# Performance work log

Hardware: AMD Instinct MI355X
Metric: run time of the kernel (lower is better)

The kernel has to match this reference:

```python
import jax, jax.numpy as jnp
import numpy as np

MARGIN = 0.3
EPS = 1e-8


def setup_inputs() -> dict:
    key = jax.random.key(0)
    k1, k2 = jax.random.split(key)
    B, D, NUM_IDS = 8192, 128, 1024
    embeddings = jax.random.normal(k1, (B, D), dtype=jnp.float32)
    labels = jax.random.randint(k2, (B,), 0, NUM_IDS, dtype=jnp.int64)
    return {"embeddings": embeddings, "labels": labels}


def _pairwise_distance(embeddings):
    # dist[i,j] = sqrt(relu(||e_i||^2 - 2 e_i.e_j + ||e_j||^2) + eps)
    dot = embeddings @ embeddings.T                       # [B, B]
    sq = jnp.diagonal(dot)                                # [B]
    d2 = sq[None, :] - 2.0 * dot + sq[:, None]
    return jnp.sqrt(jax.nn.relu(d2) + EPS)


def reference(embeddings, labels):
    B = labels.shape[0]
    dist = _pairwise_distance(embeddings)                 # [B, B]

    same = labels[:, None] == labels[None, :]             # [B, B]
    eye = jnp.eye(B, dtype=bool)
    pos_mask = same & ~eye
    neg_mask = ~same

    neg_inf = jnp.finfo(dist.dtype).min
    pos_inf = jnp.finfo(dist.dtype).max
    hardest_pos = jnp.max(jnp.where(pos_mask, dist, neg_inf), axis=1)  # [B]
    hardest_neg = jnp.min(jnp.where(neg_mask, dist, pos_inf), axis=1)  # [B]

    valid = pos_mask.any(axis=1) & neg_mask.any(axis=1)   # [B]
    per_anchor = jax.nn.relu(hardest_pos - hardest_neg + MARGIN)
    loss_sum = jnp.sum(jnp.where(valid, per_anchor, 0.0))
    n_triplets = jnp.sum(valid)
    return loss_sum / jnp.maximum(n_triplets, 1).astype(loss_sum.dtype)
```

## Files before the change

kernel.cpp:

```cpp
#include <hip/hip_runtime.h>

#define BSZ 8192
#define DIM 128
#define NLAB 1024
#define MARGIN 0.3f
#define EPS 1e-8f
#define NJ 32
#define JCHUNK 256
#define NPH 8

typedef __bf16 bf16x8 __attribute__((ext_vector_type(8)));
typedef float f32x4 __attribute__((ext_vector_type(4)));

#define AS1 __attribute__((address_space(1)))
#define AS3 __attribute__((address_space(3)))

__device__ __forceinline__ unsigned enc_ord(float f) {
    unsigned u = __float_as_uint(f);
    return (u & 0x80000000u) ? ~u : (u | 0x80000000u);
}
__device__ __forceinline__ float dec_ord(unsigned e) {
    unsigned u = (e & 0x80000000u) ? (e & 0x7FFFFFFFu) : ~e;
    return __uint_as_float(u);
}

template <int N>
__device__ __forceinline__ void waitv() {
    if constexpr (N == 4) asm volatile("s_waitcnt vmcnt(4)" ::: "memory");
    else if constexpr (N == 2) asm volatile("s_waitcnt vmcnt(2)" ::: "memory");
    else asm volatile("s_waitcnt vmcnt(0)" ::: "memory");
}

__global__ __launch_bounds__(1024) void k_sort(const int* __restrict__ labels,
                                               unsigned* __restrict__ start,
                                               unsigned* __restrict__ offset) {
    __shared__ unsigned h[NLAB];
    const int tid = threadIdx.x;
    h[tid] = 0u;
    __syncthreads();
#pragma unroll
    for (int s = 0; s < BSZ / NLAB; ++s)
        atomicAdd(&h[labels[s * NLAB + tid]], 1u);
    __syncthreads();
    for (int d = 1; d < NLAB; d <<= 1) {
        unsigned w = (tid >= d) ? h[tid - d] : 0u;
        __syncthreads();
        h[tid] += w;
        __syncthreads();
    }
    start[tid + 1] = h[tid];
    if (tid == 0) start[0] = 0u;
    offset[tid] = (tid > 0) ? h[tid - 1] : 0u;
}

__global__ __launch_bounds__(256) void k_scatter(const int* __restrict__ labels,
                                                 unsigned* __restrict__ offset,
                                                 int* __restrict__ perm,
                                                 int* __restrict__ slab) {
    int i = blockIdx.x * 256 + threadIdx.x;
    int lab = labels[i];
    unsigned pos = atomicAdd(&offset[lab], 1u);
    perm[pos] = i;
    slab[pos] = lab;
}

__global__ __launch_bounds__(256) void k_prep(const float* __restrict__ emb,
                                              const int* __restrict__ perm,
                                              __bf16* __restrict__ hi,
                                              float* __restrict__ sq,
                                              unsigned* __restrict__ maxp,
                                              unsigned* __restrict__ minn,
                                              float* __restrict__ sumcnt) {
    int row = blockIdx.x * 4 + (threadIdx.x >> 6);
    int lane = threadIdx.x & 63;
    int src = perm[row];
    float2 v = *(const float2*)&emb[(size_t)src * DIM + lane * 2];
    union { __bf16 b[2]; unsigned u; } p;
    p.b[0] = (__bf16)v.x;
    p.b[1] = (__bf16)v.y;
    ((unsigned*)hi)[row * 64 + lane] = p.u;
    float s = v.x * v.x + v.y * v.y;
#pragma unroll
    for (int m = 32; m >= 1; m >>= 1) s += __shfl_xor(s, m);
    if (lane == 0) {
        sq[row] = s;
        maxp[row] = 0u;
        minn[row] = 0xFFFFFFFFu;
    }
    if (blockIdx.x == 0 && threadIdx.x == 0) {
        sumcnt[0] = 0.0f;
        ((unsigned*)sumcnt)[1] = 0u;
    }
}

__global__ __launch_bounds__(256, 4) void k_mfma(const __bf16* __restrict__ hi,
                                                 const int* __restrict__ slab,
                                                 const unsigned* __restrict__ startp,
                                                 const float* __restrict__ sq,
                                                 unsigned* __restrict__ maxp,
                                                 unsigned* __restrict__ minn) {
    __shared__ char Bst[4][8][1024];
    __shared__ float sqlds[JCHUNK];
    __shared__ int lablds[JCHUNK];

    const int tid = threadIdx.x;
    const int lane = tid & 63;
    const int wave = tid >> 6;
    const int lr = lane & 15;
    const int lq = lane >> 4;
    const int i0 = blockIdx.x * 128;
    const int it0 = i0 + wave * 32;
    const int it1 = it0 + 16;
    const int j0 = blockIdx.y * JCHUNK;
    const float INF = __uint_as_float(0x7F800000u);

    const int lf = slab[i0];
    const int ll = slab[i0 + 127];
    const int blo = (int)startp[lf];
    const int bhi = (int)startp[ll + 1];
    unsigned mmask = 0;
#pragma unroll
    for (int tt = 0; tt < NPH; ++tt) {
        int c0 = j0 + tt * 32;
        if (bhi > c0 && blo < c0 + 32) mmask |= (1u << tt);
    }

    sqlds[tid] = sq[j0 + tid];
    lablds[tid] = slab[j0 + tid];

    bf16x8 a0[4], a1[4];
    const __bf16* ap = hi + (size_t)(it0 + lr) * DIM + lq * 8;
#pragma unroll
    for (int f = 0; f < 4; ++f) {
        a0[f] = *(const bf16x8*)&ap[f * 32];
        a1[f] = *(const bf16x8*)&ap[16 * DIM + f * 32];
        asm volatile("" : "+v"(a0[f]));
        asm volatile("" : "+v"(a1[f]));
    }
    const int4 li0 = *(const int4*)&slab[it0 + lq * 4];
    const int4 li1 = *(const int4*)&slab[it1 + lq * 4];
    const int labi0[4] = {li0.x, li0.y, li0.z, li0.w};
    const int labi1[4] = {li1.x, li1.y, li1.z, li1.w};

    float mp0[4], mp1[4], mn0[4], mn1[4];
#pragma unroll
    for (int r = 0; r < 4; ++r) {
        mp0[r] = -INF; mp1[r] = -INF;
        mn0[r] = INF;  mn1[r] = INF;
    }

    const int m0 = wave * 2, m1 = m0 + 1;
    const __bf16* bsA = hi + (size_t)(j0 + (m0 >> 2) * 16 + lr) * DIM + (m0 & 3) * 32 + lq * 8;
    const __bf16* bsB = hi + (size_t)(j0 + (m1 >> 2) * 16 + lr) * DIM + (m1 & 3) * 32 + lq * 8;
#define STAGE(t, buf)                                                              \
    do {                                                                           \
        __builtin_amdgcn_global_load_lds(                                          \
            (const AS1 void*)(bsA + (size_t)(t) * 32 * DIM),                       \
            (AS3 void*)&Bst[buf][m0][0], 16, 0, 0);                                \
        __builtin_amdgcn_global_load_lds(                                          \
            (const AS1 void*)(bsB + (size_t)(t) * 32 * DIM),                       \
            (AS3 void*)&Bst[buf][m1][0], 16, 0, 0);                                \
    } while (0)

    STAGE(0, 0);
    STAGE(1, 1);
    __syncthreads();

#pragma unroll 1
    for (int t = 0; t < NPH; ++t) {
        if (t + 2 < NPH) STAGE(t + 2, (t + 2) & 3);
        if (t < NPH - 2) waitv<4>();
        else if (t == NPH - 2) waitv<2>();
        else waitv<0>();
        __builtin_amdgcn_s_barrier();
        __builtin_amdgcn_sched_barrier(0);

        const float sqj0 = sqlds[t * 32 + lr];
        const float sqj1 = sqlds[t * 32 + 16 + lr];

        const bf16x8* bp = (const bf16x8*)&Bst[t & 3][0][0];
        f32x4 acc00 = {0, 0, 0, 0}, acc01 = {0, 0, 0, 0};
        f32x4 acc10 = {0, 0, 0, 0}, acc11 = {0, 0, 0, 0};
#pragma unroll
        for (int f = 0; f < 4; ++f) {
            bf16x8 b0 = bp[f * 64 + lane];
            bf16x8 b1 = bp[(4 + f) * 64 + lane];
            acc00 = __builtin_amdgcn_mfma_f32_16x16x32_bf16(a0[f], b0, acc00, 0, 0, 0);
            acc10 = __builtin_amdgcn_mfma_f32_16x16x32_bf16(a1[f], b0, acc10, 0, 0, 0);
            acc01 = __builtin_amdgcn_mfma_f32_16x16x32_bf16(a0[f], b1, acc01, 0, 0, 0);
            acc11 = __builtin_amdgcn_mfma_f32_16x16x32_bf16(a1[f], b1, acc11, 0, 0, 0);
        }

        if (mmask & (1u << t)) {
            const int labj0 = lablds[t * 32 + lr];
            const int labj1 = lablds[t * 32 + 16 + lr];
#pragma unroll
            for (int r = 0; r < 4; ++r) {
                float k00 = fmaf(-2.0f, acc00[r], sqj0);
                float k01 = fmaf(-2.0f, acc01[r], sqj1);
                float k10 = fmaf(-2.0f, acc10[r], sqj0);
                float k11 = fmaf(-2.0f, acc11[r], sqj1);
                bool s00 = (labj0 == labi0[r]);
                bool s01 = (labj1 == labi0[r]);
                bool s10 = (labj0 == labi1[r]);
                bool s11 = (labj1 == labi1[r]);
                mp0[r] = s00 ? fmaxf(mp0[r], k00) : mp0[r];
                mn0[r] = s00 ? mn0[r] : fminf(mn0[r], k00);
                mp0[r] = s01 ? fmaxf(mp0[r], k01) : mp0[r];
                mn0[r] = s01 ? mn0[r] : fminf(mn0[r], k01);
                mp1[r] = s10 ? fmaxf(mp1[r], k10) : mp1[r];
                mn1[r] = s10 ? mn1[r] : fminf(mn1[r], k10);
                mp1[r] = s11 ? fmaxf(mp1[r], k11) : mp1[r];
                mn1[r] = s11 ? mn1[r] : fminf(mn1[r], k11);
            }
        } else {
#pragma unroll
            for (int r = 0; r < 4; ++r) {
                float k00 = fmaf(-2.0f, acc00[r], sqj0);
                float k01 = fmaf(-2.0f, acc01[r], sqj1);
                float k10 = fmaf(-2.0f, acc10[r], sqj0);
                float k11 = fmaf(-2.0f, acc11[r], sqj1);
                mn0[r] = fminf(fminf(mn0[r], k00), k01);
                mn1[r] = fminf(fminf(mn1[r], k10), k11);
            }
        }
    }
#undef STAGE

#pragma unroll
    for (int m = 1; m < 16; m <<= 1) {
#pragma unroll
        for (int r = 0; r < 4; ++r) {
            mp0[r] = fmaxf(mp0[r], __shfl_xor(mp0[r], m));
            mn0[r] = fminf(mn0[r], __shfl_xor(mn0[r], m));
            mp1[r] = fmaxf(mp1[r], __shfl_xor(mp1[r], m));
            mn1[r] = fminf(mn1[r], __shfl_xor(mn1[r], m));
        }
    }
    if (lr == 0) {
#pragma unroll
        for (int r = 0; r < 4; ++r) {
            atomicMax(&maxp[it0 + lq * 4 + r], enc_ord(mp0[r]));
            atomicMin(&minn[it0 + lq * 4 + r], enc_ord(mn0[r]));
            atomicMax(&maxp[it1 + lq * 4 + r], enc_ord(mp1[r]));
            atomicMin(&minn[it1 + lq * 4 + r], enc_ord(mn1[r]));
        }
    }
}

__global__ __launch_bounds__(256) void k_final(const unsigned* __restrict__ maxp,
                                               const unsigned* __restrict__ minn,
                                               const float* __restrict__ sq,
                                               float* __restrict__ sumcnt) {
    int i = blockIdx.x * 256 + threadIdx.x;
    float mpd = dec_ord(maxp[i]);
    float mnd = dec_ord(minn[i]);
    float sqi = sq[i];
    bool valid = (mpd > -1e30f) && (mnd < 1e30f);
    float hp = sqrtf(fmaxf(sqi + mpd, 0.0f) + EPS);
    float hn = sqrtf(fmaxf(sqi + mnd, 0.0f) + EPS);
    float per = valid ? fmaxf(hp - hn + MARGIN, 0.0f) : 0.0f;
    unsigned cnt = valid ? 1u : 0u;
#pragma unroll
    for (int m = 32; m >= 1; m >>= 1) {
        per += __shfl_xor(per, m);
        cnt += __shfl_xor(cnt, m);
    }
    __shared__ float ssum[4];
    __shared__ unsigned scnt[4];
    int wid = threadIdx.x >> 6;
    if ((threadIdx.x & 63) == 0) { ssum[wid] = per; scnt[wid] = cnt; }
    __syncthreads();
    if (threadIdx.x == 0) {
        float s = ssum[0] + ssum[1] + ssum[2] + ssum[3];
        unsigned c = scnt[0] + scnt[1] + scnt[2] + scnt[3];
        atomicAdd(&sumcnt[0], s);
        atomicAdd((unsigned*)&sumcnt[1], c);
    }
}

__global__ void k_out(const float* __restrict__ sumcnt, float* __restrict__ out) {
    if (threadIdx.x == 0) {
        float s = sumcnt[0];
        unsigned c = ((const unsigned*)sumcnt)[1];
        out[0] = s / (float)(c > 0u ? c : 1u);
    }
}

extern "C" void kernel_launch(void* const* d_in, const int* in_sizes, int n_in,
                              void* d_out, int out_size, void* d_ws, size_t ws_size,
                              hipStream_t stream) {
    const float* emb    = (const float*)d_in[0];
    const int*   labels = (const int*)d_in[1];

    float* wsf = (float*)d_ws;
    __bf16*   hi     = (__bf16*)wsf;
    float*    sq     = wsf + 524288;
    unsigned* maxp   = (unsigned*)(wsf + 532480);
    unsigned* minn   = (unsigned*)(wsf + 540672);
    float*    sumcnt = wsf + 548864;
    unsigned* start  = (unsigned*)(wsf + 548868);
    unsigned* offset = (unsigned*)(wsf + 549896);
    int*      perm   = (int*)(wsf + 550920);
    int*      slab   = (int*)(wsf + 559112);
    float*    out    = (float*)d_out;

    k_sort<<<dim3(1), dim3(1024), 0, stream>>>(labels, start, offset);
    k_scatter<<<dim3(BSZ / 256), dim3(256), 0, stream>>>(labels, offset, perm, slab);
    k_prep<<<dim3(BSZ / 4), dim3(256), 0, stream>>>(emb, perm, hi, sq, maxp, minn, sumcnt);
    k_mfma<<<dim3(BSZ / 128, NJ), dim3(256), 0, stream>>>(hi, slab, start, sq, maxp, minn);
    k_final<<<dim3(BSZ / 256), dim3(256), 0, stream>>>(maxp, minn, sq, sumcnt);
    k_out<<<dim3(1), dim3(64), 0, stream>>>(sumcnt, out);
}
```

Baseline: 53.63 us.

## Fuse scatter into prep and fold final division into reduction kernel

Merges the label scatter into the embedding conversion kernel: each row atomically claims its sorted slot and writes the bf16 row, squared norm, label and init values directly at that slot. The final-output kernel is removed by using a last-block ticket in the reduction kernel. The histogram kernel now loads labels with vectorized int4 reads. This cuts two launches and the perm indirection, and in exchange moves the slot atomics onto the conversion path and makes within-label ordering nondeterministic.

```diff
diff --git a/kernel.cpp b/kernel.cpp
--- a/kernel.cpp
+++ b/kernel.cpp
@@ -31,16 +31,22 @@
     else asm volatile("s_waitcnt vmcnt(0)" ::: "memory");
 }
 
-__global__ __launch_bounds__(1024) void k_sort(const int* __restrict__ labels,
-                                               unsigned* __restrict__ start,
-                                               unsigned* __restrict__ offset) {
+__global__ __launch_bounds__(1024) void k_histscan(const int* __restrict__ labels,
+                                                   unsigned* __restrict__ start,
+                                                   unsigned* __restrict__ offset,
+                                                   unsigned* __restrict__ ticket,
+                                                   float* __restrict__ sumcnt) {
     __shared__ unsigned h[NLAB];
     const int tid = threadIdx.x;
     h[tid] = 0u;
     __syncthreads();
-#pragma unroll
-    for (int s = 0; s < BSZ / NLAB; ++s)
-        atomicAdd(&h[labels[s * NLAB + tid]], 1u);
+    const int4* l4 = (const int4*)labels;
+    int4 a = l4[tid];
+    int4 b = l4[tid + 1024];
+    atomicAdd(&h[a.x], 1u); atomicAdd(&h[a.y], 1u);
+    atomicAdd(&h[a.z], 1u); atomicAdd(&h[a.w], 1u);
+    atomicAdd(&h[b.x], 1u); atomicAdd(&h[b.y], 1u);
+    atomicAdd(&h[b.z], 1u); atomicAdd(&h[b.w], 1u);
     __syncthreads();
     for (int d = 1; d < NLAB; d <<= 1) {
         unsigned w = (tid >= d) ? h[tid - d] : 0u;
@@ -49,47 +55,42 @@
         __syncthreads();
     }
     start[tid + 1] = h[tid];
-    if (tid == 0) start[0] = 0u;
     offset[tid] = (tid > 0) ? h[tid - 1] : 0u;
-}
-
-__global__ __launch_bounds__(256) void k_scatter(const int* __restrict__ labels,
-                                                 unsigned* __restrict__ offset,
-                                                 int* __restrict__ perm,
-                                                 int* __restrict__ slab) {
-    int i = blockIdx.x * 256 + threadIdx.x;
-    int lab = labels[i];
-    unsigned pos = atomicAdd(&offset[lab], 1u);
-    perm[pos] = i;
-    slab[pos] = lab;
-}
-
-__global__ __launch_bounds__(256) void k_prep(const float* __restrict__ emb,
-                                              const int* __restrict__ perm,
-                                              __bf16* __restrict__ hi,
-                                              float* __restrict__ sq,
-                                              unsigned* __restrict__ maxp,
-                                              unsigned* __restrict__ minn,
-                                              float* __restrict__ sumcnt) {
+    if (tid == 0) {
+        start[0] = 0u;
+        ticket[0] = 0u;
+        sumcnt[0] = 0.0f;
+        ((unsigned*)sumcnt)[1] = 0u;
+    }
+}
+
+__global__ __launch_bounds__(256) void k_gather(const float* __restrict__ emb,
+                                                const int* __restrict__ labels,
+                                                unsigned* __restrict__ offset,
+                                                __bf16* __restrict__ hi,
+                                                float* __restrict__ sq,
+                                                int* __restrict__ slab,
+                                                unsigned* __restrict__ maxp,
+                                                unsigned* __restrict__ minn) {
     int row = blockIdx.x * 4 + (threadIdx.x >> 6);
     int lane = threadIdx.x & 63;
-    int src = perm[row];
-    float2 v = *(const float2*)&emb[(size_t)src * DIM + lane * 2];
+    int lab = labels[row];
+    unsigned pos = 0;
+    if (lane == 0) pos = atomicAdd(&offset[lab], 1u);
+    pos = __shfl(pos, 0);
+    float2 v = *(const float2*)&emb[(size_t)row * DIM + lane * 2];
     union { __bf16 b[2]; unsigned u; } p;
     p.b[0] = (__bf16)v.x;
     p.b[1] = (__bf16)v.y;
-    ((unsigned*)hi)[row * 64 + lane] = p.u;
+    ((unsigned*)hi)[pos * 64 + lane] = p.u;
     float s = v.x * v.x + v.y * v.y;
 #pragma unroll
     for (int m = 32; m >= 1; m >>= 1) s += __shfl_xor(s, m);
     if (lane == 0) {
-        sq[row] = s;
-        maxp[row] = 0u;
-        minn[row] = 0xFFFFFFFFu;
-    }
-    if (blockIdx.x == 0 && threadIdx.x == 0) {
-        sumcnt[0] = 0.0f;
-        ((unsigned*)sumcnt)[1] = 0u;
+        sq[pos] = s;
+        slab[pos] = lab;
+        maxp[pos] = 0u;
+        minn[pos] = 0xFFFFFFFFu;
     }
 }
 
@@ -251,7 +252,9 @@
 __global__ __launch_bounds__(256) void k_final(const unsigned* __restrict__ maxp,
                                                const unsigned* __restrict__ minn,
                                                const float* __restrict__ sq,
-                                               float* __restrict__ sumcnt) {
+                                               float* __restrict__ sumcnt,
+                                               unsigned* __restrict__ ticket,
+                                               float* __restrict__ out) {
     int i = blockIdx.x * 256 + threadIdx.x;
     float mpd = dec_ord(maxp[i]);
     float mnd = dec_ord(minn[i]);
@@ -276,14 +279,13 @@
         unsigned c = scnt[0] + scnt[1] + scnt[2] + scnt[3];
         atomicAdd(&sumcnt[0], s);
         atomicAdd((unsigned*)&sumcnt[1], c);
-    }
-}
-
-__global__ void k_out(const float* __restrict__ sumcnt, float* __restrict__ out) {
-    if (threadIdx.x == 0) {
-        float s = sumcnt[0];
-        unsigned c = ((const unsigned*)sumcnt)[1];
-        out[0] = s / (float)(c > 0u ? c : 1u);
+        __threadfence();
+        unsigned done = atomicAdd(ticket, 1u);
+        if (done == gridDim.x - 1) {
+            float ts = atomicAdd(&sumcnt[0], 0.0f);
+            unsigned tc = atomicAdd((unsigned*)&sumcnt[1], 0u);
+            out[0] = ts / (float)(tc > 0u ? tc : 1u);
+        }
     }
 }
 
@@ -301,14 +303,12 @@
     float*    sumcnt = wsf + 548864;
     unsigned* start  = (unsigned*)(wsf + 548868);
     unsigned* offset = (unsigned*)(wsf + 549896);
-    int*      perm   = (int*)(wsf + 550920);
-    int*      slab   = (int*)(wsf + 559112);
+    unsigned* ticket = (unsigned*)(wsf + 550920);
+    int*      slab   = (int*)(wsf + 550924);
     float*    out    = (float*)d_out;
 
-    k_sort<<<dim3(1), dim3(1024), 0, stream>>>(labels, start, offset);
-    k_scatter<<<dim3(BSZ / 256), dim3(256), 0, stream>>>(labels, offset, perm, slab);
-    k_prep<<<dim3(BSZ / 4), dim3(256), 0, stream>>>(emb, perm, hi, sq, maxp, minn, sumcnt);
+    k_histscan<<<dim3(1), dim3(1024), 0, stream>>>(labels, start, offset, ticket, sumcnt);
+    k_gather<<<dim3(BSZ / 4), dim3(256), 0, stream>>>(emb, labels, offset, hi, sq, slab, maxp, minn);
     k_mfma<<<dim3(BSZ / 128, NJ), dim3(256), 0, stream>>>(hi, slab, start, sq, maxp, minn);
-    k_final<<<dim3(BSZ / 256), dim3(256), 0, stream>>>(maxp, minn, sq, sumcnt);
-    k_out<<<dim3(1), dim3(64), 0, stream>>>(sumcnt, out);
-}
+    k_final<<<dim3(BSZ / 256), dim3(256), 0, stream>>>(maxp, minn, sq, sumcnt, ticket, out);
+}
```

After: 51.42 us. 4.1% less time.
